# Kernel tuning notes

Hardware: AMD Instinct MI355X
Metric: run time of the kernel (lower is better)

The kernel has to match this reference:

```python
import jax, jax.numpy as jnp
import numpy as np

WINDOW = (8, 8)
NUM_HEADS = 6
PAD_H, PAD_W = WINDOW[0] // 2, WINDOW[1] // 2


def window_partition(x, wh, ww):
    # x: (B, C, H, W) -> (B*nh*nw, wh*ww, C)
    B, C, H, W = x.shape
    nh, nw = H // wh, W // ww
    x = x.reshape(B, C, nh, wh, nw, ww)
    x = x.transpose(0, 2, 4, 3, 5, 1)  # B, nh, nw, wh, ww, C
    return x.reshape(B * nh * nw, wh * ww, C)


def window_merge(x, B, C, H, W, wh, ww):
    # x: (B*nh*nw, wh*ww, C) -> (B, C, H, W)
    nh, nw = H // wh, W // ww
    x = x.reshape(B, nh, nw, wh, ww, C)
    x = x.transpose(0, 5, 1, 3, 2, 4)  # B, C, nh, wh, nw, ww
    return x.reshape(B, C, H, W)


def window_mha(t, num_heads):
    # t: (Bn, N, 3*C) packed qkv -> (Bn, N, C)
    Bn, N, C3 = t.shape
    C = C3 // 3
    d = C // num_heads
    q, k, v = jnp.split(t, 3, axis=-1)
    to_heads = lambda u: u.reshape(Bn, N, num_heads, d).transpose(0, 2, 1, 3)
    q, k, v = to_heads(q), to_heads(k), to_heads(v)
    scale = 1.0 / np.sqrt(d)
    attn = jax.nn.softmax(jnp.einsum('bhnd,bhmd->bhnm', q, k) * scale, axis=-1)
    o = jnp.einsum('bhnm,bhmd->bhnd', attn, v)
    return o.transpose(0, 2, 1, 3).reshape(Bn, N, C)


def setup_inputs() -> dict:
    key = jax.random.key(0)
    ks = jax.random.split(key, 5)
    B, C, H, W = 4, 384, 128, 128
    Cq = 64 * NUM_HEADS  # qkv_dim * num_heads = 384
    return {
        'x': jax.random.normal(ks[0], (B, C, H, W), dtype=jnp.float32),
        'w_qkv': jax.random.normal(ks[1], (3 * Cq, C), dtype=jnp.float32) * 0.02,
        'b_qkv': jax.random.normal(ks[2], (3 * Cq,), dtype=jnp.float32) * 0.02,
        'w_head': jax.random.normal(ks[3], (C, Cq), dtype=jnp.float32) * 0.02,
        'b_head': jax.random.normal(ks[4], (C,), dtype=jnp.float32) * 0.02,
    }


def reference(x, w_qkv, b_qkv, w_head, b_head):
    B, C, H, W = x.shape
    wh, ww = WINDOW
    # 1x1 conv qkv projection
    qkv = jnp.einsum('bchw,oc->bohw', x, w_qkv) + b_qkv[None, :, None, None]
    Cq = qkv.shape[1] // 3
    # branch 1: unpadded windows
    x1 = window_partition(qkv, wh, ww)
    x1 = window_mha(x1, NUM_HEADS)
    x1 = window_merge(x1, B, Cq, H, W, wh, ww)
    # branch 2: pad by half window, windows, then crop back
    qkv_p = jnp.pad(qkv, ((0, 0), (0, 0), (PAD_H, PAD_H), (PAD_W, PAD_W)))
    Hp, Wp = H + 2 * PAD_H, W + 2 * PAD_W
    x2 = window_partition(qkv_p, wh, ww)
    x2 = window_mha(x2, NUM_HEADS)
    x2 = window_merge(x2, B, Cq, Hp, Wp, wh, ww)
    x2 = x2[:, :, PAD_H:Hp - PAD_H, PAD_W:Wp - PAD_W]
    # merge + 1x1 conv head projection
    out = jnp.einsum('bchw,oc->bohw', x1 + x2, w_head) + b_head[None, :, None, None]
    return out
```

## Files before the change

### kernel.cpp

```cpp
#include <hip/hip_runtime.h>

typedef __bf16 bf16x8 __attribute__((ext_vector_type(8)));
typedef float f32x4 __attribute__((ext_vector_type(4)));

#define HW 16384
#define SP 66

union U4B8 { uint4 u; bf16x8 v; __bf16 h[8]; };
union U2B4 { uint2 u; __bf16 h[4]; };

__device__ __forceinline__ void gload_lds16(const __bf16* g, __bf16* l) {
    __builtin_amdgcn_global_load_lds(
        (const __attribute__((address_space(1))) unsigned int*)g,
        (__attribute__((address_space(3))) unsigned int*)l, 16, 0, 0);
}

__global__ __launch_bounds__(256) void k_xt(const float* __restrict__ x,
    __bf16* __restrict__ xT)
{
    __shared__ __bf16 T[64 * 68];
    const int tid = threadIdx.x;
    const int hw0 = blockIdx.x * 64;
    const int c0  = blockIdx.y * 64;
    const int b   = blockIdx.z;
    const float* xb = x + (size_t)b * 384 * HW;
#pragma unroll
    for (int it = 0; it < 4; ++it) {
        int unit = it * 256 + tid;
        int c = unit >> 4, q = unit & 15;
        float4 f = *(const float4*)(xb + (size_t)(c0 + c) * HW + hw0 + q * 4);
        U2B4 t;
        t.h[0] = (__bf16)f.x; t.h[1] = (__bf16)f.y;
        t.h[2] = (__bf16)f.z; t.h[3] = (__bf16)f.w;
        *(uint2*)(T + c * 68 + q * 4) = t.u;
    }
    __syncthreads();
    __bf16* xtb = xT + (size_t)b * HW * 384;
#pragma unroll
    for (int it = 0; it < 2; ++it) {
        int unit = it * 256 + tid;
        int hw = unit >> 3, c8 = unit & 7;
        U4B8 t;
#pragma unroll
        for (int j = 0; j < 8; ++j) t.h[j] = T[(c8 * 8 + j) * 68 + hw];
        *(uint4*)(xtb + (size_t)(hw0 + hw) * 384 + c0 + c8 * 8) = t.u;
    }
}

__global__ __launch_bounds__(256) void k_cvt(const float* __restrict__ src,
    __bf16* __restrict__ dst)
{
    int idx = (blockIdx.x * 256 + threadIdx.x) * 8;
    float4 f0 = *(const float4*)(src + idx);
    float4 f1 = *(const float4*)(src + idx + 4);
    U4B8 t;
    t.h[0] = (__bf16)f0.x; t.h[1] = (__bf16)f0.y;
    t.h[2] = (__bf16)f0.z; t.h[3] = (__bf16)f0.w;
    t.h[4] = (__bf16)f1.x; t.h[5] = (__bf16)f1.y;
    t.h[6] = (__bf16)f1.z; t.h[7] = (__bf16)f1.w;
    *(uint4*)(dst + idx) = t.u;
}

__global__ __launch_bounds__(256) void k_qkv(const __bf16* __restrict__ xT,
    const __bf16* __restrict__ wqb, const float* __restrict__ bq,
    __bf16* __restrict__ qk, __bf16* __restrict__ vT)
{
    __shared__ __bf16 As[128 * 64];
    __shared__ __bf16 Bs[128 * 64];
    const int tid = threadIdx.x;
    const int hw0 = blockIdx.x * 128;
    const int o0  = blockIdx.y * 128;
    const int b   = blockIdx.z;

    f32x4 acc[4][4];
#pragma unroll
    for (int i = 0; i < 4; ++i)
#pragma unroll
        for (int j = 0; j < 4; ++j)
#pragma unroll
            for (int e = 0; e < 4; ++e) acc[i][j][e] = 0.0f;

    const int l = tid & 63;
    const int wv = tid >> 6;
    const int wm = wv & 1;
    const int wn = wv >> 1;
    const int l16 = l & 15, quad = l >> 4;

    const __bf16* wrow = wqb + (size_t)o0 * 384;
    const __bf16* xrow = xT + (size_t)b * HW * 384 + (size_t)hw0 * 384;
    const int r = tid >> 3, c8 = (tid & 7) * 8;

    for (int kt = 0; kt < 6; ++kt) {
        const int c0 = kt * 64;
#pragma unroll
        for (int it = 0; it < 4; ++it) {
            int unit = it * 256 + tid;
            int rr = r + it * 32;
            gload_lds16(wrow + (size_t)rr * 384 + c0 + c8, As + unit * 8);
            gload_lds16(xrow + (size_t)rr * 384 + c0 + c8, Bs + unit * 8);
        }
        __syncthreads();
#pragma unroll
        for (int ks = 0; ks < 2; ++ks) {
            bf16x8 a[4], bb[4];
#pragma unroll
            for (int t = 0; t < 4; ++t)
                a[t] = *(const bf16x8*)(As + (wm * 64 + t * 16 + l16) * 64 + ks * 32 + quad * 8);
#pragma unroll
            for (int t = 0; t < 4; ++t)
                bb[t] = *(const bf16x8*)(Bs + (wn * 64 + t * 16 + l16) * 64 + ks * 32 + quad * 8);
#pragma unroll
            for (int mt = 0; mt < 4; ++mt)
#pragma unroll
                for (int nt = 0; nt < 4; ++nt)
                    acc[mt][nt] = __builtin_amdgcn_mfma_f32_16x16x32_bf16(
                        a[mt], bb[nt], acc[mt][nt], 0, 0, 0);
        }
        __syncthreads();
    }

    if (o0 < 768) {
        __bf16* qb = qk + (size_t)b * HW * 768;
#pragma unroll
        for (int mt = 0; mt < 4; ++mt) {
            int oo = o0 + wm * 64 + mt * 16 + quad * 4;
            float4 bias = *(const float4*)(bq + oo);
#pragma unroll
            for (int nt = 0; nt < 4; ++nt) {
                int hw = hw0 + wn * 64 + nt * 16 + l16;
                U2B4 t;
                t.h[0] = (__bf16)(acc[mt][nt][0] + bias.x);
                t.h[1] = (__bf16)(acc[mt][nt][1] + bias.y);
                t.h[2] = (__bf16)(acc[mt][nt][2] + bias.z);
                t.h[3] = (__bf16)(acc[mt][nt][3] + bias.w);
                *(uint2*)(qb + (size_t)hw * 768 + oo) = t.u;
            }
        }
    } else {
        __bf16* vb = vT + (size_t)b * 384 * HW;
#pragma unroll
        for (int mt = 0; mt < 4; ++mt) {
            int oo = o0 + wm * 64 + mt * 16 + quad * 4;
            float4 bias = *(const float4*)(bq + oo);
            int vo = oo - 768;
#pragma unroll
            for (int nt = 0; nt < 4; ++nt) {
                int hw = hw0 + wn * 64 + nt * 16 + l16;
                vb[(size_t)(vo + 0) * HW + hw] = (__bf16)(acc[mt][nt][0] + bias.x);
                vb[(size_t)(vo + 1) * HW + hw] = (__bf16)(acc[mt][nt][1] + bias.y);
                vb[(size_t)(vo + 2) * HW + hw] = (__bf16)(acc[mt][nt][2] + bias.z);
                vb[(size_t)(vo + 3) * HW + hw] = (__bf16)(acc[mt][nt][3] + bias.w);
            }
        }
    }
}

__global__ __launch_bounds__(192) void k_attn(const __bf16* __restrict__ qk,
    const __bf16* __restrict__ vT, __bf16* __restrict__ y1,
    __bf16* __restrict__ y2)
{
    __shared__ __bf16 sm[3][64 * SP];
    const int tid = threadIdx.x;
    const int l = tid & 63, wv = tid >> 6;
    const int wid = blockIdx.x * 3 + wv;
    const bool shifted = wid >= 6144;
    const int w2 = shifted ? wid - 6144 : wid;
    const int head = w2 % 6;
    const int win = w2 / 6;
    const int nw = shifted ? 17 : 16;
    const int wx = win % nw;
    const int t2 = win / nw;
    const int wy = t2 % nw;
    const int b  = t2 / nw;
    const int h0 = wy * 8 - (shifted ? 4 : 0);
    const int w0 = wx * 8 - (shifted ? 4 : 0);
    const __bf16* qb = qk + (size_t)b * HW * 768;
    const __bf16* vb = vT + (size_t)b * 384 * HW;
    __bf16* P = &sm[wv][0];
    const int l16 = l & 15, quad = l >> 4;
    const int cbase = head * 64;

    size_t toff[4]; bool tval[4];
#pragma unroll
    for (int t = 0; t < 4; ++t) {
        int tok = t * 16 + l16;
        int hh = h0 + (tok >> 3), ww = w0 + (tok & 7);
        tval[t] = ((unsigned)hh < 128u && (unsigned)ww < 128u);
        toff[t] = tval[t] ? (size_t)(hh * 128 + ww) * 768 : 0;
    }

    f32x4 s[4][4];
#pragma unroll
    for (int i = 0; i < 4; ++i)
#pragma unroll
        for (int j = 0; j < 4; ++j)
#pragma unroll
            for (int e = 0; e < 4; ++e) s[i][j][e] = 0.0f;

#pragma unroll
    for (int ks = 0; ks < 2; ++ks) {
        bf16x8 aq[4], bk[4];
#pragma unroll
        for (int t = 0; t < 4; ++t) {
            U4B8 uq, uk;
            if (tval[t]) {
                uq.u = *(const uint4*)(qb + toff[t] + cbase + ks * 32 + quad * 8);
                uk.u = *(const uint4*)(qb + toff[t] + 384 + cbase + ks * 32 + quad * 8);
            } else {
                uq.u = make_uint4(0, 0, 0, 0);
                uk.u = make_uint4(0, 0, 0, 0);
            }
            aq[t] = uq.v;
            bk[t] = uk.v;
        }
        __builtin_amdgcn_s_setprio(1);
#pragma unroll
        for (int mt = 0; mt < 4; ++mt)
#pragma unroll
            for (int nt = 0; nt < 4; ++nt)
                s[mt][nt] = __builtin_amdgcn_mfma_f32_16x16x32_bf16(
                    aq[mt], bk[nt], s[mt][nt], 0, 0, 0);
        __builtin_amdgcn_s_setprio(0);
    }

#pragma unroll
    for (int mt = 0; mt < 4; ++mt) {
#pragma unroll
        for (int e = 0; e < 4; ++e) {
            float p[4];
#pragma unroll
            for (int nt = 0; nt < 4; ++nt) p[nt] = __expf(s[mt][nt][e] * 0.125f);
            float sum = (p[0] + p[1]) + (p[2] + p[3]);
#pragma unroll
            for (int st = 1; st < 16; st <<= 1) sum += __shfl_xor(sum, st, 64);
            float r = __fdividef(1.0f, sum);
            int row = mt * 16 + quad * 4 + e;
#pragma unroll
            for (int nt = 0; nt < 4; ++nt)
                P[row * SP + nt * 16 + l16] = (__bf16)(p[nt] * r);
        }
    }

    f32x4 o[4][4];
#pragma unroll
    for (int i = 0; i < 4; ++i)
#pragma unroll
        for (int j = 0; j < 4; ++j)
#pragma unroll
            for (int e = 0; e < 4; ++e) o[i][j][e] = 0.0f;

#pragma unroll
    for (int ks = 0; ks < 2; ++ks) {
        bf16x8 ap[4], bvv[4];
#pragma unroll
        for (int t = 0; t < 4; ++t)
            ap[t] = *(const bf16x8*)(P + (t * 16 + l16) * SP + ks * 32 + quad * 8);
        const int th = ks * 4 + quad;
        const int hh2 = h0 + th;
        const bool rowok = ((unsigned)hh2 < 128u);
#pragma unroll
        for (int t = 0; t < 4; ++t) {
            U4B8 u;
            u.u = make_uint4(0, 0, 0, 0);
            if (rowok) {
                const __bf16* vp = vb + (size_t)(cbase + t * 16 + l16) * HW
                                   + (hh2 * 128 + w0);
                if (!shifted) {
                    u.u = *(const uint4*)vp;
                } else {
                    if (w0 >= 0)   *(uint2*)&u.h[0] = *(const uint2*)vp;
                    if (w0 <= 120) *(uint2*)&u.h[4] = *(const uint2*)(vp + 4);
                }
            }
            bvv[t] = u.v;
        }
        __builtin_amdgcn_s_setprio(1);
#pragma unroll
        for (int mt = 0; mt < 4; ++mt)
#pragma unroll
            for (int nt = 0; nt < 4; ++nt)
                o[mt][nt] = __builtin_amdgcn_mfma_f32_16x16x32_bf16(
                    ap[mt], bvv[nt], o[mt][nt], 0, 0, 0);
        __builtin_amdgcn_s_setprio(0);
    }

#pragma unroll
    for (int mt = 0; mt < 4; ++mt)
#pragma unroll
        for (int e = 0; e < 4; ++e) {
            int row = mt * 16 + quad * 4 + e;
#pragma unroll
            for (int nt = 0; nt < 4; ++nt)
                P[row * SP + nt * 16 + l16] = (__bf16)o[mt][nt][e];
        }

    __bf16* yb = (shifted ? y2 : y1) + (size_t)b * HW * 384;
#pragma unroll
    for (int it = 0; it < 8; ++it) {
        int unit = it * 64 + l;
        int tok = unit >> 3, c8 = unit & 7;
        int hh = h0 + (tok >> 3), ww = w0 + (tok & 7);
        if ((unsigned)hh < 128u && (unsigned)ww < 128u)
            *(uint4*)(yb + (size_t)(hh * 128 + ww) * 384 + cbase + c8 * 8) =
                *(const uint4*)(P + tok * SP + c8 * 8);
    }
}

__global__ __launch_bounds__(256) void k_ysum(const __bf16* __restrict__ y1,
    const __bf16* __restrict__ y2, __bf16* __restrict__ ysum)
{
    int idx = (blockIdx.x * 256 + threadIdx.x) * 8;
    U4B8 t1, t2, r;
    t1.u = *(const uint4*)(y1 + idx);
    t2.u = *(const uint4*)(y2 + idx);
#pragma unroll
    for (int e = 0; e < 8; ++e)
        r.h[e] = (__bf16)((float)t1.h[e] + (float)t2.h[e]);
    *(uint4*)(ysum + idx) = r.u;
}

__global__ __launch_bounds__(256) void k_head(const __bf16* __restrict__ ysum,
    const __bf16* __restrict__ whb, const float* __restrict__ bh,
    float* __restrict__ out)
{
    __shared__ __bf16 As[128 * 64];
    __shared__ __bf16 Bs[128 * 64];
    const int tid = threadIdx.x;
    const int hw0 = blockIdx.x * 128;
    const int o0  = blockIdx.y * 128;
    const int b   = blockIdx.z;

    f32x4 acc[4][4];
#pragma unroll
    for (int i = 0; i < 4; ++i)
#pragma unroll
        for (int j = 0; j < 4; ++j)
#pragma unroll
            for (int e = 0; e < 4; ++e) acc[i][j][e] = 0.0f;

    const int l = tid & 63, wv = tid >> 6;
    const int wm = wv & 1;
    const int wn = wv >> 1;
    const int l16 = l & 15, quad = l >> 4;

    const __bf16* yrow = ysum + (size_t)b * HW * 384 + (size_t)hw0 * 384;
    const __bf16* wrow = whb + (size_t)o0 * 384;
    const int r = tid >> 3, c8 = (tid & 7) * 8;

    for (int kt = 0; kt < 6; ++kt) {
        const int c0 = kt * 64;
#pragma unroll
        for (int it = 0; it < 4; ++it) {
            int unit = it * 256 + tid;
            int rr = r + it * 32;
            gload_lds16(yrow + (size_t)rr * 384 + c0 + c8, As + unit * 8);
            gload_lds16(wrow + (size_t)rr * 384 + c0 + c8, Bs + unit * 8);
        }
        __syncthreads();
#pragma unroll
        for (int ks = 0; ks < 2; ++ks) {
            bf16x8 a[4], bb[4];
#pragma unroll
            for (int t = 0; t < 4; ++t)
                a[t] = *(const bf16x8*)(As + (wm * 64 + t * 16 + l16) * 64 + ks * 32 + quad * 8);
#pragma unroll
            for (int t = 0; t < 4; ++t)
                bb[t] = *(const bf16x8*)(Bs + (wn * 64 + t * 16 + l16) * 64 + ks * 32 + quad * 8);
#pragma unroll
            for (int mt = 0; mt < 4; ++mt)
#pragma unroll
                for (int nt = 0; nt < 4; ++nt)
                    acc[mt][nt] = __builtin_amdgcn_mfma_f32_16x16x32_bf16(
                        a[mt], bb[nt], acc[mt][nt], 0, 0, 0);
        }
        __syncthreads();
    }

#pragma unroll
    for (int nt = 0; nt < 4; ++nt) {
        int oo = o0 + wn * 64 + nt * 16 + l16;
        float bb_ = bh[oo];
        float* ob = out + ((size_t)b * 384 + oo) * HW + hw0 + wm * 64;
#pragma unroll
        for (int mt = 0; mt < 4; ++mt) {
            float4 f;
            f.x = acc[mt][nt][0] + bb_;
            f.y = acc[mt][nt][1] + bb_;
            f.z = acc[mt][nt][2] + bb_;
            f.w = acc[mt][nt][3] + bb_;
            *(float4*)(ob + mt * 16 + quad * 4) = f;
        }
    }
}

extern "C" void kernel_launch(void* const* d_in, const int* in_sizes, int n_in,
                              void* d_out, int out_size, void* d_ws, size_t ws_size,
                              hipStream_t stream) {
    const float* x  = (const float*)d_in[0];
    const float* wq = (const float*)d_in[1];
    const float* bq = (const float*)d_in[2];
    const float* wh = (const float*)d_in[3];
    const float* bh = (const float*)d_in[4];
    float* out = (float*)d_out;

    __bf16* qk = (__bf16*)d_ws;
    __bf16* vT = qk + (size_t)4 * HW * 768;
    __bf16* y1 = vT + (size_t)4 * 384 * HW;
    __bf16* y2 = y1 + (size_t)4 * HW * 384;
    __bf16* xT   = y1;
    __bf16* wqb  = y2;
    __bf16* ysum = qk;
    __bf16* whb  = vT;

    k_xt  <<<dim3(256, 6, 4), 256, 0, stream>>>(x, xT);
    k_cvt <<<dim3(216),       256, 0, stream>>>(wq, wqb);
    k_qkv <<<dim3(128, 9, 4), 256, 0, stream>>>(xT, wqb, bq, qk, vT);
    k_attn<<<dim3(4360),      192, 0, stream>>>(qk, vT, y1, y2);
    k_ysum<<<dim3(12288),     256, 0, stream>>>(y1, y2, ysum);
    k_cvt <<<dim3(72),        256, 0, stream>>>(wh, whb);
    k_head<<<dim3(128, 3, 4), 256, 0, stream>>>(ysum, whb, bh, out);
}
```

Before: 487.5 us.

## Split attention into per-branch kernels, fuse ysum into shifted pass, double-buffer GEMMs

The combined attention kernel becomes two specialised kernels. The unshifted one drops all bounds checks, and the shifted one reads y1 and writes the summed result directly, so the separate ysum elementwise kernel and the y2 buffer go away. V loads are issued before the softmax so their latency overlaps. Both 1x1-conv GEMMs now double-buffer LDS tiles so the next K tile loads while the MFMAs run. In exchange, LDS use per block doubles, which may lower occupancy, and attn2 now depends on attn1 finishing first.

```diff
diff --git a/kernel.cpp b/kernel.cpp
--- a/kernel.cpp
+++ b/kernel.cpp
@@ -65,8 +65,8 @@
     const __bf16* __restrict__ wqb, const float* __restrict__ bq,
     __bf16* __restrict__ qk, __bf16* __restrict__ vT)
 {
-    __shared__ __bf16 As[128 * 64];
-    __shared__ __bf16 Bs[128 * 64];
+    __shared__ __bf16 As[2][128 * 64];
+    __shared__ __bf16 Bs[2][128 * 64];
     const int tid = threadIdx.x;
     const int hw0 = blockIdx.x * 128;
     const int o0  = blockIdx.y * 128;
@@ -90,25 +90,31 @@
     const __bf16* xrow = xT + (size_t)b * HW * 384 + (size_t)hw0 * 384;
     const int r = tid >> 3, c8 = (tid & 7) * 8;
 
-    for (int kt = 0; kt < 6; ++kt) {
+    auto STAGE = [&](int buf, int kt) {
         const int c0 = kt * 64;
 #pragma unroll
         for (int it = 0; it < 4; ++it) {
             int unit = it * 256 + tid;
             int rr = r + it * 32;
-            gload_lds16(wrow + (size_t)rr * 384 + c0 + c8, As + unit * 8);
-            gload_lds16(xrow + (size_t)rr * 384 + c0 + c8, Bs + unit * 8);
-        }
-        __syncthreads();
+            gload_lds16(wrow + (size_t)rr * 384 + c0 + c8, &As[buf][unit * 8]);
+            gload_lds16(xrow + (size_t)rr * 384 + c0 + c8, &Bs[buf][unit * 8]);
+        }
+    };
+
+    STAGE(0, 0);
+    __syncthreads();
+    int cur = 0;
+    for (int kt = 0; kt < 6; ++kt) {
+        if (kt < 5) STAGE(cur ^ 1, kt + 1);
 #pragma unroll
         for (int ks = 0; ks < 2; ++ks) {
             bf16x8 a[4], bb[4];
 #pragma unroll
             for (int t = 0; t < 4; ++t)
-                a[t] = *(const bf16x8*)(As + (wm * 64 + t * 16 + l16) * 64 + ks * 32 + quad * 8);
+                a[t] = *(const bf16x8*)(&As[cur][(wm * 64 + t * 16 + l16) * 64 + ks * 32 + quad * 8]);
 #pragma unroll
             for (int t = 0; t < 4; ++t)
-                bb[t] = *(const bf16x8*)(Bs + (wn * 64 + t * 16 + l16) * 64 + ks * 32 + quad * 8);
+                bb[t] = *(const bf16x8*)(&Bs[cur][(wn * 64 + t * 16 + l16) * 64 + ks * 32 + quad * 8]);
 #pragma unroll
             for (int mt = 0; mt < 4; ++mt)
 #pragma unroll
@@ -116,7 +122,8 @@
                     acc[mt][nt] = __builtin_amdgcn_mfma_f32_16x16x32_bf16(
                         a[mt], bb[nt], acc[mt][nt], 0, 0, 0);
         }
-        __syncthreads();
+        if (kt < 5) __syncthreads();
+        cur ^= 1;
     }
 
     if (o0 < 768) {
@@ -155,25 +162,150 @@
     }
 }
 
-__global__ __launch_bounds__(192) void k_attn(const __bf16* __restrict__ qk,
-    const __bf16* __restrict__ vT, __bf16* __restrict__ y1,
-    __bf16* __restrict__ y2)
+__global__ __launch_bounds__(192) void k_attn1(const __bf16* __restrict__ qk,
+    const __bf16* __restrict__ vT, __bf16* __restrict__ y1)
 {
     __shared__ __bf16 sm[3][64 * SP];
     const int tid = threadIdx.x;
     const int l = tid & 63, wv = tid >> 6;
     const int wid = blockIdx.x * 3 + wv;
-    const bool shifted = wid >= 6144;
-    const int w2 = shifted ? wid - 6144 : wid;
-    const int head = w2 % 6;
-    const int win = w2 / 6;
-    const int nw = shifted ? 17 : 16;
-    const int wx = win % nw;
-    const int t2 = win / nw;
-    const int wy = t2 % nw;
-    const int b  = t2 / nw;
-    const int h0 = wy * 8 - (shifted ? 4 : 0);
-    const int w0 = wx * 8 - (shifted ? 4 : 0);
+    const int head = wid % 6;
+    const int win = wid / 6;
+    const int wx = win & 15;
+    const int wy = (win >> 4) & 15;
+    const int b  = win >> 8;
+    const int h0 = wy * 8, w0 = wx * 8;
+    const __bf16* qb = qk + (size_t)b * HW * 768;
+    const __bf16* vb = vT + (size_t)b * 384 * HW;
+    __bf16* P = &sm[wv][0];
+    const int l16 = l & 15, quad = l >> 4;
+    const int cbase = head * 64;
+
+    size_t toff[4];
+#pragma unroll
+    for (int t = 0; t < 4; ++t) {
+        int tok = t * 16 + l16;
+        toff[t] = (size_t)((h0 + (tok >> 3)) * 128 + w0 + (tok & 7)) * 768;
+    }
+
+    f32x4 s[4][4];
+#pragma unroll
+    for (int i = 0; i < 4; ++i)
+#pragma unroll
+        for (int j = 0; j < 4; ++j)
+#pragma unroll
+            for (int e = 0; e < 4; ++e) s[i][j][e] = 0.0f;
+
+#pragma unroll
+    for (int ks = 0; ks < 2; ++ks) {
+        bf16x8 aq[4], bk[4];
+#pragma unroll
+        for (int t = 0; t < 4; ++t) {
+            U4B8 uq, uk;
+            uq.u = *(const uint4*)(qb + toff[t] + cbase + ks * 32 + quad * 8);
+            uk.u = *(const uint4*)(qb + toff[t] + 384 + cbase + ks * 32 + quad * 8);
+            aq[t] = uq.v;
+            bk[t] = uk.v;
+        }
+        __builtin_amdgcn_s_setprio(1);
+#pragma unroll
+        for (int mt = 0; mt < 4; ++mt)
+#pragma unroll
+            for (int nt = 0; nt < 4; ++nt)
+                s[mt][nt] = __builtin_amdgcn_mfma_f32_16x16x32_bf16(
+                    aq[mt], bk[nt], s[mt][nt], 0, 0, 0);
+        __builtin_amdgcn_s_setprio(0);
+    }
+
+    U4B8 vreg[2][4];
+#pragma unroll
+    for (int ks = 0; ks < 2; ++ks) {
+        const int hh2 = h0 + ks * 4 + quad;
+#pragma unroll
+        for (int t = 0; t < 4; ++t)
+            vreg[ks][t].u = *(const uint4*)(vb +
+                (size_t)(cbase + t * 16 + l16) * HW + (hh2 * 128 + w0));
+    }
+
+#pragma unroll
+    for (int mt = 0; mt < 4; ++mt) {
+#pragma unroll
+        for (int e = 0; e < 4; ++e) {
+            float p[4];
+#pragma unroll
+            for (int nt = 0; nt < 4; ++nt) p[nt] = __expf(s[mt][nt][e] * 0.125f);
+            float sum = (p[0] + p[1]) + (p[2] + p[3]);
+#pragma unroll
+            for (int st = 1; st < 16; st <<= 1) sum += __shfl_xor(sum, st, 64);
+            float r = __fdividef(1.0f, sum);
+            int row = mt * 16 + quad * 4 + e;
+#pragma unroll
+            for (int nt = 0; nt < 4; ++nt)
+                P[row * SP + nt * 16 + l16] = (__bf16)(p[nt] * r);
+        }
+    }
+
+    f32x4 o[4][4];
+#pragma unroll
+    for (int i = 0; i < 4; ++i)
+#pragma unroll
+        for (int j = 0; j < 4; ++j)
+#pragma unroll
+            for (int e = 0; e < 4; ++e) o[i][j][e] = 0.0f;
+
+#pragma unroll
+    for (int ks = 0; ks < 2; ++ks) {
+        bf16x8 ap[4];
+#pragma unroll
+        for (int t = 0; t < 4; ++t)
+            ap[t] = *(const bf16x8*)(P + (t * 16 + l16) * SP + ks * 32 + quad * 8);
+        __builtin_amdgcn_s_setprio(1);
+#pragma unroll
+        for (int mt = 0; mt < 4; ++mt)
+#pragma unroll
+            for (int nt = 0; nt < 4; ++nt)
+                o[mt][nt] = __builtin_amdgcn_mfma_f32_16x16x32_bf16(
+                    ap[mt], vreg[ks][nt].v, o[mt][nt], 0, 0, 0);
+        __builtin_amdgcn_s_setprio(0);
+    }
+
+#pragma unroll
+    for (int mt = 0; mt < 4; ++mt)
+#pragma unroll
+        for (int e = 0; e < 4; ++e) {
+            int row = mt * 16 + quad * 4 + e;
+#pragma unroll
+            for (int nt = 0; nt < 4; ++nt)
+                P[row * SP + nt * 16 + l16] = (__bf16)o[mt][nt][e];
+        }
+
+    __bf16* yb = y1 + (size_t)b * HW * 384;
+#pragma unroll
+    for (int it = 0; it < 8; ++it) {
+        int unit = it * 64 + l;
+        int tok = unit >> 3, c8 = unit & 7;
+        int hh = h0 + (tok >> 3), ww = w0 + (tok & 7);
+        *(uint4*)(yb + (size_t)(hh * 128 + ww) * 384 + cbase + c8 * 8) =
+            *(const uint4*)(P + tok * SP + c8 * 8);
+    }
+}
+
+__global__ __launch_bounds__(192) void k_attn2(const __bf16* __restrict__ qk,
+    const __bf16* __restrict__ vT, const __bf16* __restrict__ y1,
+    __bf16* __restrict__ ysum)
+{
+    __shared__ __bf16 sm[3][64 * SP];
+    const int tid = threadIdx.x;
+    const int l = tid & 63, wv = tid >> 6;
+    const int wid = blockIdx.x * 3 + wv;
+    const int head = wid % 6;
+    const int win = wid / 6;
+    const int wx = win % 17;
+    const int t2 = win / 17;
+    const int wy = t2 % 17;
+    const int b  = t2 / 17;
+    const int h0 = wy * 8 - 4;
+    const int w0 = wx * 8 - 4;
     const __bf16* qb = qk + (size_t)b * HW * 768;
     const __bf16* vb = vT + (size_t)b * 384 * HW;
     __bf16* P = &sm[wv][0];
@@ -223,40 +355,10 @@
         __builtin_amdgcn_s_setprio(0);
     }
 
-#pragma unroll
-    for (int mt = 0; mt < 4; ++mt) {
-#pragma unroll
-        for (int e = 0; e < 4; ++e) {
-            float p[4];
-#pragma unroll
-            for (int nt = 0; nt < 4; ++nt) p[nt] = __expf(s[mt][nt][e] * 0.125f);
-            float sum = (p[0] + p[1]) + (p[2] + p[3]);
-#pragma unroll
-            for (int st = 1; st < 16; st <<= 1) sum += __shfl_xor(sum, st, 64);
-            float r = __fdividef(1.0f, sum);
-            int row = mt * 16 + quad * 4 + e;
-#pragma unroll
-            for (int nt = 0; nt < 4; ++nt)
-                P[row * SP + nt * 16 + l16] = (__bf16)(p[nt] * r);
-        }
-    }
-
-    f32x4 o[4][4];
-#pragma unroll
-    for (int i = 0; i < 4; ++i)
-#pragma unroll
-        for (int j = 0; j < 4; ++j)
-#pragma unroll
-            for (int e = 0; e < 4; ++e) o[i][j][e] = 0.0f;
-
+    U4B8 vreg[2][4];
 #pragma unroll
     for (int ks = 0; ks < 2; ++ks) {
-        bf16x8 ap[4], bvv[4];
-#pragma unroll
-        for (int t = 0; t < 4; ++t)
-            ap[t] = *(const bf16x8*)(P + (t * 16 + l16) * SP + ks * 32 + quad * 8);
-        const int th = ks * 4 + quad;
-        const int hh2 = h0 + th;
+        const int hh2 = h0 + ks * 4 + quad;
         const bool rowok = ((unsigned)hh2 < 128u);
 #pragma unroll
         for (int t = 0; t < 4; ++t) {
@@ -265,22 +367,52 @@
             if (rowok) {
                 const __bf16* vp = vb + (size_t)(cbase + t * 16 + l16) * HW
                                    + (hh2 * 128 + w0);
-                if (!shifted) {
-                    u.u = *(const uint4*)vp;
-                } else {
-                    if (w0 >= 0)   *(uint2*)&u.h[0] = *(const uint2*)vp;
-                    if (w0 <= 120) *(uint2*)&u.h[4] = *(const uint2*)(vp + 4);
-                }
+                if (w0 >= 0)   *(uint2*)&u.h[0] = *(const uint2*)vp;
+                if (w0 <= 120) *(uint2*)&u.h[4] = *(const uint2*)(vp + 4);
             }
-            bvv[t] = u.v;
-        }
+            vreg[ks][t] = u;
+        }
+    }
+
+#pragma unroll
+    for (int mt = 0; mt < 4; ++mt) {
+#pragma unroll
+        for (int e = 0; e < 4; ++e) {
+            float p[4];
+#pragma unroll
+            for (int nt = 0; nt < 4; ++nt) p[nt] = __expf(s[mt][nt][e] * 0.125f);
+            float sum = (p[0] + p[1]) + (p[2] + p[3]);
+#pragma unroll
+            for (int st = 1; st < 16; st <<= 1) sum += __shfl_xor(sum, st, 64);
+            float r = __fdividef(1.0f, sum);
+            int row = mt * 16 + quad * 4 + e;
+#pragma unroll
+            for (int nt = 0; nt < 4; ++nt)
+                P[row * SP + nt * 16 + l16] = (__bf16)(p[nt] * r);
+        }
+    }
+
+    f32x4 o[4][4];
+#pragma unroll
+    for (int i = 0; i < 4; ++i)
+#pragma unroll
+        for (int j = 0; j < 4; ++j)
+#pragma unroll
+            for (int e = 0; e < 4; ++e) o[i][j][e] = 0.0f;
+
+#pragma unroll
+    for (int ks = 0; ks < 2; ++ks) {
+        bf16x8 ap[4];
+#pragma unroll
+        for (int t = 0; t < 4; ++t)
+            ap[t] = *(const bf16x8*)(P + (t * 16 + l16) * SP + ks * 32 + quad * 8);
         __builtin_amdgcn_s_setprio(1);
 #pragma unroll
         for (int mt = 0; mt < 4; ++mt)
 #pragma unroll
             for (int nt = 0; nt < 4; ++nt)
                 o[mt][nt] = __builtin_amdgcn_mfma_f32_16x16x32_bf16(
-                    ap[mt], bvv[nt], o[mt][nt], 0, 0, 0);
+                    ap[mt], vreg[ks][nt].v, o[mt][nt], 0, 0, 0);
         __builtin_amdgcn_s_setprio(0);
     }
 
@@ -294,37 +426,32 @@
                 P[row * SP + nt * 16 + l16] = (__bf16)o[mt][nt][e];
         }
 
-    __bf16* yb = (shifted ? y2 : y1) + (size_t)b * HW * 384;
+    const __bf16* y1b = y1 + (size_t)b * HW * 384;
+    __bf16* yb = ysum + (size_t)b * HW * 384;
 #pragma unroll
     for (int it = 0; it < 8; ++it) {
         int unit = it * 64 + l;
         int tok = unit >> 3, c8 = unit & 7;
         int hh = h0 + (tok >> 3), ww = w0 + (tok & 7);
-        if ((unsigned)hh < 128u && (unsigned)ww < 128u)
-            *(uint4*)(yb + (size_t)(hh * 128 + ww) * 384 + cbase + c8 * 8) =
-                *(const uint4*)(P + tok * SP + c8 * 8);
-    }
-}
-
-__global__ __launch_bounds__(256) void k_ysum(const __bf16* __restrict__ y1,
-    const __bf16* __restrict__ y2, __bf16* __restrict__ ysum)
-{
-    int idx = (blockIdx.x * 256 + threadIdx.x) * 8;
-    U4B8 t1, t2, r;
-    t1.u = *(const uint4*)(y1 + idx);
-    t2.u = *(const uint4*)(y2 + idx);
-#pragma unroll
-    for (int e = 0; e < 8; ++e)
-        r.h[e] = (__bf16)((float)t1.h[e] + (float)t2.h[e]);
-    *(uint4*)(ysum + idx) = r.u;
+        if ((unsigned)hh < 128u && (unsigned)ww < 128u) {
+            size_t off = (size_t)(hh * 128 + ww) * 384 + cbase + c8 * 8;
+            U4B8 t1, t2, r;
+            t1.u = *(const uint4*)(y1b + off);
+            t2.u = *(const uint4*)(P + tok * SP + c8 * 8);
+#pragma unroll
+            for (int e = 0; e < 8; ++e)
+                r.h[e] = (__bf16)((float)t1.h[e] + (float)t2.h[e]);
+            *(uint4*)(yb + off) = r.u;
+        }
+    }
 }
 
 __global__ __launch_bounds__(256) void k_head(const __bf16* __restrict__ ysum,
     const __bf16* __restrict__ whb, const float* __restrict__ bh,
     float* __restrict__ out)
 {
-    __shared__ __bf16 As[128 * 64];
-    __shared__ __bf16 Bs[128 * 64];
+    __shared__ __bf16 As[2][128 * 64];
+    __shared__ __bf16 Bs[2][128 * 64];
     const int tid = threadIdx.x;
     const int hw0 = blockIdx.x * 128;
     const int o0  = blockIdx.y * 128;
@@ -347,25 +474,31 @@
     const __bf16* wrow = whb + (size_t)o0 * 384;
     const int r = tid >> 3, c8 = (tid & 7) * 8;
 
-    for (int kt = 0; kt < 6; ++kt) {
+    auto STAGE = [&](int buf, int kt) {
         const int c0 = kt * 64;
 #pragma unroll
         for (int it = 0; it < 4; ++it) {
             int unit = it * 256 + tid;
             int rr = r + it * 32;
-            gload_lds16(yrow + (size_t)rr * 384 + c0 + c8, As + unit * 8);
-            gload_lds16(wrow + (size_t)rr * 384 + c0 + c8, Bs + unit * 8);
-        }
-        __syncthreads();
+            gload_lds16(yrow + (size_t)rr * 384 + c0 + c8, &As[buf][unit * 8]);
+            gload_lds16(wrow + (size_t)rr * 384 + c0 + c8, &Bs[buf][unit * 8]);
+        }
+    };
+
+    STAGE(0, 0);
+    __syncthreads();
+    int cur = 0;
+    for (int kt = 0; kt < 6; ++kt) {
+        if (kt < 5) STAGE(cur ^ 1, kt + 1);
 #pragma unroll
         for (int ks = 0; ks < 2; ++ks) {
             bf16x8 a[4], bb[4];
 #pragma unroll
             for (int t = 0; t < 4; ++t)
-                a[t] = *(const bf16x8*)(As + (wm * 64 + t * 16 + l16) * 64 + ks * 32 + quad * 8);
+                a[t] = *(const bf16x8*)(&As[cur][(wm * 64 + t * 16 + l16) * 64 + ks * 32 + quad * 8]);
 #pragma unroll
             for (int t = 0; t < 4; ++t)
-                bb[t] = *(const bf16x8*)(Bs + (wn * 64 + t * 16 + l16) * 64 + ks * 32 + quad * 8);
+                bb[t] = *(const bf16x8*)(&Bs[cur][(wn * 64 + t * 16 + l16) * 64 + ks * 32 + quad * 8]);
 #pragma unroll
             for (int mt = 0; mt < 4; ++mt)
 #pragma unroll
@@ -373,7 +506,8 @@
                     acc[mt][nt] = __builtin_amdgcn_mfma_f32_16x16x32_bf16(
                         a[mt], bb[nt], acc[mt][nt], 0, 0, 0);
         }
-        __syncthreads();
+        if (kt < 5) __syncthreads();
+        cur ^= 1;
     }
 
 #pragma unroll
@@ -406,17 +540,16 @@
     __bf16* qk = (__bf16*)d_ws;
     __bf16* vT = qk + (size_t)4 * HW * 768;
     __bf16* y1 = vT + (size_t)4 * 384 * HW;
-    __bf16* y2 = y1 + (size_t)4 * HW * 384;
+    __bf16* ys = y1 + (size_t)4 * HW * 384;
     __bf16* xT   = y1;
-    __bf16* wqb  = y2;
-    __bf16* ysum = qk;
+    __bf16* wqb  = ys;
     __bf16* whb  = vT;
 
-    k_xt  <<<dim3(256, 6, 4), 256, 0, stream>>>(x, xT);
-    k_cvt <<<dim3(216),       256, 0, stream>>>(wq, wqb);
-    k_qkv <<<dim3(128, 9, 4), 256, 0, stream>>>(xT, wqb, bq, qk, vT);
-    k_attn<<<dim3(4360),      192, 0, stream>>>(qk, vT, y1, y2);
-    k_ysum<<<dim3(12288),     256, 0, stream>>>(y1, y2, ysum);
-    k_cvt <<<dim3(72),        256, 0, stream>>>(wh, whb);
-    k_head<<<dim3(128, 3, 4), 256, 0, stream>>>(ysum, whb, bh, out);
-}
+    k_xt   <<<dim3(256, 6, 4), 256, 0, stream>>>(x, xT);
+    k_cvt  <<<dim3(216),       256, 0, stream>>>(wq, wqb);
+    k_qkv  <<<dim3(128, 9, 4), 256, 0, stream>>>(xT, wqb, bq, qk, vT);
+    k_attn1<<<dim3(2048),      192, 0, stream>>>(qk, vT, y1);
+    k_attn2<<<dim3(2312),      192, 0, stream>>>(qk, vT, y1, ys);
+    k_cvt  <<<dim3(72),        256, 0, stream>>>(wh, whb);
+    k_head <<<dim3(128, 3, 4), 256, 0, stream>>>(ys, whb, bh, out);
+}
```

New measurement: 463.2 us. 5.0% less time.
